# Performance work log

Hardware: AMD Instinct MI355X
Metric: run time of the kernel (lower is better)

The kernel has to match this reference:

```python
import jax, jax.numpy as jnp
import numpy as np

B, ENTRY, TUPLE, CLASSES = 4096, 1024, 16, 10
NEURONS = ENTRY // TUPLE            # 64, pad_bits = 0
ADDR_SPACE = 2 ** TUPLE             # 65536


def setup_inputs() -> dict:
    key = jax.random.key(0)
    k1, k2, k3 = jax.random.split(key, 3)
    # binary input bits
    samples = jax.random.randint(k1, (B, ENTRY), 0, 2, dtype=jnp.int32)
    # per-class random permutation of the (padded) entry bits
    tuple_mapping = jnp.argsort(jax.random.uniform(k2, (CLASSES, ENTRY)), axis=1).astype(jnp.int32)
    ram = (jax.random.uniform(k3, (CLASSES, NEURONS, ADDR_SPACE)) < 0.05).astype(jnp.float32)
    return {"samples": samples, "tuple_mapping": tuple_mapping, "ram": ram}


def reference(samples, tuple_mapping, ram):
    # samples: [B, E] binary int32; tuple_mapping: [C, E]; ram: [C, N, A]
    Bn = samples.shape[0]
    C, E = tuple_mapping.shape
    _, N, A = ram.shape
    T = E // N
    # per-class bit remapping (torch.index_select per class, vectorized)
    mapped = samples[:, tuple_mapping]                      # [B, C, E]
    bits = mapped.reshape(Bn, C, N, T)                      # [B, C, N, T]
    # transform: (bits << flip(arange(T))).sum -> big-endian tuple address
    weights = (2 ** jnp.flip(jnp.arange(T))).astype(jnp.int32)  # [T]
    addr = (bits * weights).sum(axis=-1)                    # [B, C, N] in [0, A)
    # RAM lookup (dense equivalent of dict lookup + isin membership)
    cidx = jnp.arange(C)[None, :, None]
    nidx = jnp.arange(N)[None, None, :]
    vals = ram[cidx, nidx, addr]                            # [B, C, N]
    # discriminator response = count of firing neurons per class
    return vals.sum(axis=-1)                                # [B, C]
```

## Files before the change

### kernel.cpp

```cpp
#include <hip/hip_runtime.h>


#define BATCH      4096
#define ENTRY      1024
#define TUPLE      16
#define CLASSES    10
#define NEURONS    64

__global__ __launch_bounds__(256) void pack_kernel(
    const int* __restrict__ samples,
    unsigned long long* __restrict__ packed64)
{
    const int gtid = blockIdx.x * 256 + threadIdx.x;
    const int wave = gtid >> 6;
    const int lane = gtid & 63;
    const int* sp = samples + (size_t)wave * ENTRY;
#pragma unroll
    for (int t = 0; t < 16; ++t) {
        int v = sp[t * 64 + lane];
        unsigned long long m = __ballot(v & 1);
        if (lane == 0) packed64[wave * 16 + t] = m;
    }
}

__global__ __launch_bounds__(256) void wisard_kernel(
    const int* __restrict__ tm,
    const float* __restrict__ ram,
    const unsigned* __restrict__ packed,
    float* __restrict__ out)
{
    const int tid  = threadIdx.x;
    const int lane = tid & 63;
    const int wid  = tid >> 6;
    const int bid  = blockIdx.x;
    const int c    = bid >> 10;
    const int s    = ((bid & 1023) << 2) | wid;

    const int4* tmp4 = reinterpret_cast<const int4*>(tm + c * ENTRY + lane * TUPLE);
    const int4 t0 = tmp4[0];
    const int4 t1 = tmp4[1];
    const int4 t2 = tmp4[2];
    const int4 t3 = tmp4[3];

    const unsigned myword = packed[s * 32 + (lane & 31)];

    unsigned addr = 0;
#define WSTEP(E)                                                 \
    {                                                            \
        const int  w_   = (E) >> 5;                              \
        const int  b_   = (E) & 31;                              \
        const unsigned word_ = (unsigned)__shfl((int)myword, w_);\
        addr = (addr << 1) | ((word_ >> b_) & 1u);               \
    }
    WSTEP(t0.x) WSTEP(t0.y) WSTEP(t0.z) WSTEP(t0.w)
    WSTEP(t1.x) WSTEP(t1.y) WSTEP(t1.z) WSTEP(t1.w)
    WSTEP(t2.x) WSTEP(t2.y) WSTEP(t2.z) WSTEP(t2.w)
    WSTEP(t3.x) WSTEP(t3.y) WSTEP(t3.z) WSTEP(t3.w)
#undef WSTEP

    const unsigned ridx = (((unsigned)(c * NEURONS + lane)) << 16) | addr;
    float v = ram[ridx];

#pragma unroll
    for (int off = 32; off > 0; off >>= 1)
        v += __shfl_xor(v, off);

    if (lane == 0) out[s * CLASSES + c] = v;
}

extern "C" void kernel_launch(void* const* d_in, const int* in_sizes, int n_in,
                              void* d_out, int out_size, void* d_ws, size_t ws_size,
                              hipStream_t stream)
{
    const int*   samples = (const int*)d_in[0];
    const int*   tm      = (const int*)d_in[1];
    const float* ram     = (const float*)d_in[2];
    float*       out     = (float*)d_out;

    unsigned long long* packed64 = (unsigned long long*)d_ws;

    pack_kernel<<<BATCH / 4, 256, 0, stream>>>(samples, packed64);

    wisard_kernel<<<CLASSES * (BATCH / 4), 256, 0, stream>>>(
        tm, ram, (const unsigned*)packed64, out);
}
```

Before: 54.52 us.

## Restructure into transpose-pack, address, bitmask-gather, and popcount reduce kernels

Replaces the two-kernel pipeline with four kernels. Samples are packed into a bit-transposed layout, and 16-bit addresses are computed per (class, neuron). Each neuron's RAM row is streamed in full and compressed into a 64-bit-word bitmask in shared memory, so lookups hit LDS instead of making random global reads. Per-neuron hit bits are stored as ballots and popcounted in a final reduce. This trades random 4-byte gathers over a 168MB table for a full sequential read of it, at the cost of extra launches and intermediate buffers.

```diff
diff --git a/kernel.cpp b/kernel.cpp
--- a/kernel.cpp
+++ b/kernel.cpp
@@ -1,71 +1,143 @@
 #include <hip/hip_runtime.h>
 
 
-#define BATCH      4096
-#define ENTRY      1024
-#define TUPLE      16
-#define CLASSES    10
-#define NEURONS    64
+#define BATCH   4096
+#define ENTRY   1024
+#define TUPLE   16
+#define CLASSES 10
+#define NEURONS 64
+#define CN      (CLASSES * NEURONS)
+#define ADDRSP  65536
 
-__global__ __launch_bounds__(256) void pack_kernel(
-    const int* __restrict__ samples,
-    unsigned long long* __restrict__ packed64)
+typedef unsigned long long u64;
+typedef unsigned int       u32;
+typedef unsigned short     u16;
+
+__global__ __launch_bounds__(256) void packT_kernel(
+    const int* __restrict__ samples, u64* __restrict__ bitT)
 {
-    const int gtid = blockIdx.x * 256 + threadIdx.x;
-    const int wave = gtid >> 6;
-    const int lane = gtid & 63;
-    const int* sp = samples + (size_t)wave * ENTRY;
+    const int b    = blockIdx.x;
+    const int sg   = b >> 4;
+    const int j16  = b & 15;
+    const int w    = threadIdx.x >> 6;
+    const int lane = threadIdx.x & 63;
+    const int j0   = j16 * 64 + w * 16;
+    const int* rp  = samples + (size_t)(sg * 64 + lane) * ENTRY;
 #pragma unroll
-    for (int t = 0; t < 16; ++t) {
-        int v = sp[t * 64 + lane];
-        unsigned long long m = __ballot(v & 1);
-        if (lane == 0) packed64[wave * 16 + t] = m;
+    for (int k = 0; k < 4; ++k) {
+        const int j = j0 + k * 4;
+        const int4 v = *reinterpret_cast<const int4*>(rp + j);
+        const u64 m0 = __ballot(v.x & 1);
+        const u64 m1 = __ballot(v.y & 1);
+        const u64 m2 = __ballot(v.z & 1);
+        const u64 m3 = __ballot(v.w & 1);
+        if (lane == 0) {
+            bitT[(j + 0) * 64 + sg] = m0;
+            bitT[(j + 1) * 64 + sg] = m1;
+            bitT[(j + 2) * 64 + sg] = m2;
+            bitT[(j + 3) * 64 + sg] = m3;
+        }
     }
 }
 
-__global__ __launch_bounds__(256) void wisard_kernel(
-    const int* __restrict__ tm,
-    const float* __restrict__ ram,
-    const unsigned* __restrict__ packed,
-    float* __restrict__ out)
+__global__ __launch_bounds__(256) void addr_kernel(
+    const int* __restrict__ tm, const u64* __restrict__ bitT,
+    u16* __restrict__ addrT)
 {
-    const int tid  = threadIdx.x;
-    const int lane = tid & 63;
-    const int wid  = tid >> 6;
-    const int bid  = blockIdx.x;
-    const int c    = bid >> 10;
-    const int s    = ((bid & 1023) << 2) | wid;
+    const int b    = blockIdx.x;
+    const int cn   = b >> 4;
+    const int sgq  = b & 15;
+    const int w    = threadIdx.x >> 6;
+    const int lane = threadIdx.x & 63;
+    const int sg   = sgq * 4 + w;
+    const int c    = cn >> 6;
+    const int n    = cn & 63;
 
-    const int4* tmp4 = reinterpret_cast<const int4*>(tm + c * ENTRY + lane * TUPLE);
-    const int4 t0 = tmp4[0];
-    const int4 t1 = tmp4[1];
-    const int4 t2 = tmp4[2];
-    const int4 t3 = tmp4[3];
+    const int* tp = tm + c * ENTRY + n * TUPLE;
+    const int4 i0 = reinterpret_cast<const int4*>(tp)[0];
+    const int4 i1 = reinterpret_cast<const int4*>(tp)[1];
+    const int4 i2 = reinterpret_cast<const int4*>(tp)[2];
+    const int4 i3 = reinterpret_cast<const int4*>(tp)[3];
 
-    const unsigned myword = packed[s * 32 + (lane & 31)];
+    u32 addr = 0;
+#define ASTEP(E)                                                   \
+    {                                                              \
+        const u64 word_ = bitT[(E) * 64 + sg];                     \
+        addr = (addr << 1) | (u32)((word_ >> lane) & 1ull);        \
+    }
+    ASTEP(i0.x) ASTEP(i0.y) ASTEP(i0.z) ASTEP(i0.w)
+    ASTEP(i1.x) ASTEP(i1.y) ASTEP(i1.z) ASTEP(i1.w)
+    ASTEP(i2.x) ASTEP(i2.y) ASTEP(i2.z) ASTEP(i2.w)
+    ASTEP(i3.x) ASTEP(i3.y) ASTEP(i3.z) ASTEP(i3.w)
+#undef ASTEP
 
-    unsigned addr = 0;
-#define WSTEP(E)                                                 \
-    {                                                            \
-        const int  w_   = (E) >> 5;                              \
-        const int  b_   = (E) & 31;                              \
-        const unsigned word_ = (unsigned)__shfl((int)myword, w_);\
-        addr = (addr << 1) | ((word_ >> b_) & 1u);               \
+    addrT[cn * BATCH + sg * 64 + lane] = (u16)addr;
+}
+
+__global__ __launch_bounds__(256) void gather_kernel(
+    const float* __restrict__ ram, const u16* __restrict__ addrT,
+    u64* __restrict__ partial)
+{
+    __shared__ u64 tbl[512];
+    const int b    = blockIdx.x;
+    const int cn   = b >> 1;
+    const int h    = b & 1;
+    const int w    = threadIdx.x >> 6;
+    const int lane = threadIdx.x & 63;
+
+    const float4* rp = reinterpret_cast<const float4*>(
+        ram + (size_t)cn * ADDRSP + h * 32768);
+
+#pragma unroll 8
+    for (int i = 0; i < 32; ++i) {
+        const int g = w * 32 + i;
+        const float4 v = rp[g * 64 + lane];
+        const u64 m0 = __ballot(v.x != 0.0f);
+        const u64 m1 = __ballot(v.y != 0.0f);
+        const u64 m2 = __ballot(v.z != 0.0f);
+        const u64 m3 = __ballot(v.w != 0.0f);
+        if (lane == 0) {
+            tbl[g * 4 + 0] = m0;
+            tbl[g * 4 + 1] = m1;
+            tbl[g * 4 + 2] = m2;
+            tbl[g * 4 + 3] = m3;
+        }
     }
-    WSTEP(t0.x) WSTEP(t0.y) WSTEP(t0.z) WSTEP(t0.w)
-    WSTEP(t1.x) WSTEP(t1.y) WSTEP(t1.z) WSTEP(t1.w)
-    WSTEP(t2.x) WSTEP(t2.y) WSTEP(t2.z) WSTEP(t2.w)
-    WSTEP(t3.x) WSTEP(t3.y) WSTEP(t3.z) WSTEP(t3.w)
-#undef WSTEP
+    __syncthreads();
 
-    const unsigned ridx = (((unsigned)(c * NEURONS + lane)) << 16) | addr;
-    float v = ram[ridx];
+    const u16* ap = addrT + cn * BATCH;
+    u64* pp = partial + (size_t)(cn * 2 + h) * 64;
+#pragma unroll
+    for (int i = 0; i < 16; ++i) {
+        const int sidx = w * 1024 + i * 64 + lane;
+        const u32 a     = ap[sidx];
+        const u32 local = a & 32767u;
+        const u64 word  = tbl[(local >> 8) * 4 + (a & 3u)];
+        u32 bit = (u32)(word >> ((local >> 2) & 63u)) & 1u;
+        bit &= (u32)((a >> 15) == (u32)h);
+        const u64 m = __ballot(bit != 0u);
+        if (lane == 0) pp[w * 16 + i] = m;
+    }
+}
 
+__global__ __launch_bounds__(256) void reduce_kernel(
+    const u64* __restrict__ partial, float* __restrict__ out)
+{
+    const int gid  = blockIdx.x * 4 + (threadIdx.x >> 6);
+    const int lane = threadIdx.x & 63;
+    const int c    = gid >> 6;
+    const int sg   = gid & 63;
+
+    const u64* pp = partial + (size_t)((c * NEURONS + lane) * 2) * 64 + sg;
+    const u64 m = pp[0] | pp[64];
+
+    float myv = 0.0f;
 #pragma unroll
-    for (int off = 32; off > 0; off >>= 1)
-        v += __shfl_xor(v, off);
-
-    if (lane == 0) out[s * CLASSES + c] = v;
+    for (int b2 = 0; b2 < 64; ++b2) {
+        const u64 mb = __ballot((u32)(m >> b2) & 1u);
+        if (lane == b2) myv = (float)__popcll(mb);
+    }
+    out[(sg * 64 + lane) * CLASSES + c] = myv;
 }
 
 extern "C" void kernel_launch(void* const* d_in, const int* in_sizes, int n_in,
@@ -77,10 +149,12 @@
     const float* ram     = (const float*)d_in[2];
     float*       out     = (float*)d_out;
 
-    unsigned long long* packed64 = (unsigned long long*)d_ws;
+    u64* bitT    = (u64*)d_ws;
+    u16* addrT   = (u16*)((char*)d_ws + (512u << 10));
+    u64* partial = (u64*)((char*)d_ws + (512u << 10) + CN * BATCH * sizeof(u16));
 
-    pack_kernel<<<BATCH / 4, 256, 0, stream>>>(samples, packed64);
-
-    wisard_kernel<<<CLASSES * (BATCH / 4), 256, 0, stream>>>(
-        tm, ram, (const unsigned*)packed64, out);
+    packT_kernel <<<1024, 256, 0, stream>>>(samples, bitT);
+    addr_kernel  <<<CN * 16, 256, 0, stream>>>(tm, bitT, addrT);
+    gather_kernel<<<CN * 2, 256, 0, stream>>>(ram, addrT, partial);
+    reduce_kernel<<<CN / 4, 256, 0, stream>>>(partial, out);
 }
```

After: 67.85 us. 24.4% more time.
